# Kernel tuning notes

Measured on AMD Instinct MI355X. Metric: run time of the kernel, lower is better.

## Reference

```python
import jax, jax.numpy as jnp
import numpy as np

NUM_HEADS = 16
D_MODEL = 1024
D_K = 64
D_V = 64
NEG_INF = -1e9


def setup_inputs() -> dict:
    key = jax.random.key(0)
    ks = jax.random.split(key, 7)
    B, S = 2, 2048
    Q = jax.random.normal(ks[0], (B, S, D_MODEL), dtype=jnp.float32)
    K = jax.random.normal(ks[1], (B, S, D_MODEL), dtype=jnp.float32)
    V = jax.random.normal(ks[2], (B, S, D_MODEL), dtype=jnp.float32)
    s = 1.0 / np.sqrt(D_MODEL)
    W_q = jax.random.normal(ks[3], (D_MODEL, D_K * NUM_HEADS), dtype=jnp.float32) * s
    W_k = jax.random.normal(ks[4], (D_MODEL, D_K), dtype=jnp.float32) * s
    W_v = jax.random.normal(ks[5], (D_MODEL, D_V), dtype=jnp.float32) * s
    W_o = jax.random.normal(ks[6], (D_V * NUM_HEADS, D_MODEL), dtype=jnp.float32) * (1.0 / np.sqrt(D_V * NUM_HEADS))
    return {"Q": Q, "K": K, "V": V, "W_q": W_q, "W_k": W_k, "W_v": W_v, "W_o": W_o}


def reference(Q, K, V, W_q, W_k, W_v, W_o):
    B, Sq, _ = Q.shape
    Sk = K.shape[1]
    # projections: Q -> per-head, K/V -> single shared head (MQA)
    q = (Q @ W_q).reshape(B, Sq, NUM_HEADS, D_K).transpose(0, 2, 1, 3)  # [B,H,Sq,Dk]
    k = K @ W_k  # [B,Sk,Dk]
    v = V @ W_v  # [B,Sk,Dv]
    scores = jnp.einsum('bhqd,bkd->bhqk', q, k) / jnp.sqrt(jnp.float32(D_K))
    causal = jnp.tril(jnp.ones((Sq, Sk), dtype=bool))  # [Sq,Sk]
    scores = jnp.where(causal[None, None], scores, NEG_INF)
    attn = jax.nn.softmax(scores, axis=-1)  # [B,H,Sq,Sk]
    out = jnp.einsum('bhqk,bkd->bhqd', attn, v)  # [B,H,Sq,Dv]
    out = out.transpose(0, 2, 1, 3).reshape(B, Sq, NUM_HEADS * D_V)
    return out @ W_o
```

## Files before the change

### kernel.cpp

```cpp
#include <hip/hip_runtime.h>
#include <hip/hip_bf16.h>
#include <cstdint>

typedef __bf16 bf16_t;
typedef __bf16 bf16x8 __attribute__((ext_vector_type(8)));
typedef __bf16 bf16x4 __attribute__((ext_vector_type(4)));
typedef float  floatx4 __attribute__((ext_vector_type(4)));

__device__ __forceinline__ bf16_t f2bf(float x) { return (bf16_t)x; }

__device__ __forceinline__ void gll16(const void* g, void* l) {
  __builtin_amdgcn_global_load_lds((const __attribute__((address_space(1))) void*)g,
                                   (__attribute__((address_space(3))) void*)l, 16, 0, 0);
}

#define S_LEN 2048
#define NHEAD 16

__global__ __launch_bounds__(256) void transpose_all(const float* __restrict__ Wq,
                                                     const float* __restrict__ Wo,
                                                     const float* __restrict__ Wk,
                                                     const float* __restrict__ Wv,
                                                     bf16_t* __restrict__ Wqt,
                                                     bf16_t* __restrict__ Wot,
                                                     bf16_t* __restrict__ Wkt,
                                                     bf16_t* __restrict__ Wvt) {
  const int bid = blockIdx.x;
  const float* W; bf16_t* Wt; int n0, k0, N;
  if (bid < 2048) {
    int z = bid >> 10, rem = bid & 1023;
    W = z ? Wo : Wq; Wt = z ? Wot : Wqt;
    n0 = (rem & 31) * 32; k0 = (rem >> 5) * 32; N = 1024;
  } else {
    int b2 = bid - 2048, z = b2 >> 6, rem = b2 & 63;
    W = z ? Wv : Wk; Wt = z ? Wvt : Wkt;
    n0 = (rem & 1) * 32; k0 = (rem >> 1) * 32; N = 64;
  }
  const int K = 1024;
  __shared__ float tile[32][33];
  int tx = threadIdx.x & 31, ty = threadIdx.x >> 5;
#pragma unroll
  for (int r = 0; r < 4; ++r)
    tile[ty + 8 * r][tx] = W[(size_t)(k0 + ty + 8 * r) * N + n0 + tx];
  __syncthreads();
#pragma unroll
  for (int r = 0; r < 4; ++r)
    Wt[(size_t)(n0 + ty + 8 * r) * K + k0 + tx] = f2bf(tile[tx][ty + 8 * r]);
}

template <int OUTMODE, bool A_FP32>
__device__ __forceinline__ void gemm_body(const void* __restrict__ Ain,
                                          const bf16_t* __restrict__ Bt,
                                          void* __restrict__ Cout,
                                          int M, int N, int K,
                                          int m0, int n0,
                                          bf16_t* As, bf16_t* Bs) {
  constexpr int BK = 64;
  const int tid = threadIdx.x;
  const int wave = tid >> 6, lane = tid & 63;
  const int quad = lane >> 4, lm = lane & 15;
  const int wr = wave >> 1, wc = wave & 1;

  floatx4 acc[2][4];
#pragma unroll
  for (int i = 0; i < 2; ++i)
#pragma unroll
    for (int j = 0; j < 4; ++j) acc[i][j] = (floatx4){0.f, 0.f, 0.f, 0.f};

  for (int k0 = 0; k0 < K; k0 += BK) {
    if constexpr (A_FP32) {
#pragma unroll
      for (int rd = 0; rd < 2; ++rd) {
        int idx = rd * 256 + tid, row = idx >> 3, ch = (idx & 7) ^ (row & 7);
        const float* src = (const float*)Ain + (size_t)(m0 + row) * K + k0 + ch * 8;
        float4 f0 = *(const float4*)src;
        float4 f1 = *(const float4*)(src + 4);
        bf16x8 o;
        o[0] = f2bf(f0.x); o[1] = f2bf(f0.y); o[2] = f2bf(f0.z); o[3] = f2bf(f0.w);
        o[4] = f2bf(f1.x); o[5] = f2bf(f1.y); o[6] = f2bf(f1.z); o[7] = f2bf(f1.w);
        *(bf16x8*)&As[idx * 8] = o;
      }
    } else {
#pragma unroll
      for (int rd = 0; rd < 2; ++rd) {
        int idx = rd * 256 + tid, row = idx >> 3, ch = (idx & 7) ^ (row & 7);
        gll16((const bf16_t*)Ain + (size_t)(m0 + row) * K + k0 + ch * 8,
              As + (rd * 256 + wave * 64) * 8);
      }
    }
#pragma unroll
    for (int rd = 0; rd < 4; ++rd) {
      int idx = rd * 256 + tid, row = idx >> 3, ch = (idx & 7) ^ (row & 7);
      gll16(Bt + (size_t)(n0 + row) * K + k0 + ch * 8,
            Bs + (rd * 256 + wave * 64) * 8);
    }
    __syncthreads();
    const int sw = lm & 7;
    bf16x8 af[2][2], bfr[4][2];
#pragma unroll
    for (int i = 0; i < 2; ++i) {
      const bf16_t* base = &As[(wr * 32 + i * 16 + lm) * BK];
      af[i][0] = *(const bf16x8*)(base + ((quad ^ sw) * 8));
      af[i][1] = *(const bf16x8*)(base + (((4 + quad) ^ sw) * 8));
    }
#pragma unroll
    for (int j = 0; j < 4; ++j) {
      const bf16_t* base = &Bs[(wc * 64 + j * 16 + lm) * BK];
      bfr[j][0] = *(const bf16x8*)(base + ((quad ^ sw) * 8));
      bfr[j][1] = *(const bf16x8*)(base + (((4 + quad) ^ sw) * 8));
    }
#pragma unroll
    for (int ks = 0; ks < 2; ++ks)
#pragma unroll
      for (int i = 0; i < 2; ++i)
#pragma unroll
        for (int j = 0; j < 4; ++j)
          acc[i][j] = __builtin_amdgcn_mfma_f32_16x16x32_bf16(af[i][ks], bfr[j][ks],
                                                              acc[i][j], 0, 0, 0);
    __syncthreads();
  }
#pragma unroll
  for (int i = 0; i < 2; ++i) {
#pragma unroll
    for (int j = 0; j < 4; ++j) {
      int row0 = m0 + wr * 32 + i * 16 + quad * 4;
      int col = n0 + wc * 64 + j * 16 + lm;
#pragma unroll
      for (int r = 0; r < 4; ++r) {
        if constexpr (OUTMODE == 3)
          ((bf16_t*)Cout)[(size_t)(row0 + r) * N + col] = f2bf(acc[i][j][r] * 0.125f);
        else
          ((float*)Cout)[(size_t)(row0 + r) * N + col] = acc[i][j][r];
      }
    }
  }
}

__device__ __forceinline__ void kv_body(const float* __restrict__ A32,
                                        const bf16_t* __restrict__ Bt,
                                        bf16_t* __restrict__ kp,
                                        bf16_t* __restrict__ vpt,
                                        int M, int K, int m0, int isV,
                                        bf16_t* As, bf16_t* Bs) {
  constexpr int BK = 32, LDK = 40, N = 64;
  const int tid = threadIdx.x;
  const int wave = tid >> 6, lane = tid & 63;
  const int quad = lane >> 4, lm = lane & 15;
  const int wr = wave >> 1, wc = wave & 1;

  floatx4 acc[2][2];
#pragma unroll
  for (int i = 0; i < 2; ++i)
#pragma unroll
    for (int j = 0; j < 2; ++j) acc[i][j] = (floatx4){0.f, 0.f, 0.f, 0.f};

  for (int k0 = 0; k0 < K; k0 += BK) {
    {
      int row = tid >> 2, c8 = tid & 3;
      const float* src = A32 + (size_t)(m0 + row) * K + k0 + c8 * 8;
      float4 f0 = *(const float4*)src;
      float4 f1 = *(const float4*)(src + 4);
      bf16x8 o;
      o[0] = f2bf(f0.x); o[1] = f2bf(f0.y); o[2] = f2bf(f0.z); o[3] = f2bf(f0.w);
      o[4] = f2bf(f1.x); o[5] = f2bf(f1.y); o[6] = f2bf(f1.z); o[7] = f2bf(f1.w);
      *(bf16x8*)&As[row * LDK + c8 * 8] = o;
    }
    {
      int row = tid >> 2, c8 = tid & 3;
      *(bf16x8*)&Bs[row * LDK + c8 * 8] =
          *(const bf16x8*)(Bt + (size_t)row * K + k0 + c8 * 8);
    }
    __syncthreads();
    bf16x8 af[2], bfr[2];
#pragma unroll
    for (int i = 0; i < 2; ++i)
      af[i] = *(const bf16x8*)&As[(wr * 32 + i * 16 + lm) * LDK + quad * 8];
#pragma unroll
    for (int j = 0; j < 2; ++j)
      bfr[j] = *(const bf16x8*)&Bs[(wc * 32 + j * 16 + lm) * LDK + quad * 8];
#pragma unroll
    for (int i = 0; i < 2; ++i)
#pragma unroll
      for (int j = 0; j < 2; ++j)
        acc[i][j] = __builtin_amdgcn_mfma_f32_16x16x32_bf16(af[i], bfr[j],
                                                            acc[i][j], 0, 0, 0);
    __syncthreads();
  }
#pragma unroll
  for (int i = 0; i < 2; ++i) {
#pragma unroll
    for (int j = 0; j < 2; ++j) {
      int row0 = m0 + wr * 32 + i * 16 + quad * 4;
      int col = wc * 32 + j * 16 + lm;
      if (isV) {
        bf16x4 o;
#pragma unroll
        for (int r = 0; r < 4; ++r) o[r] = f2bf(acc[i][j][r]);
        *(bf16x4*)&vpt[(size_t)col * M + row0] = o;
      } else {
#pragma unroll
        for (int r = 0; r < 4; ++r)
          kp[(size_t)(row0 + r) * N + col] = f2bf(acc[i][j][r]);
      }
    }
  }
}

__global__ __launch_bounds__(256, 2) void proj_all(const float* __restrict__ Q,
                                                   const float* __restrict__ K,
                                                   const float* __restrict__ V,
                                                   const bf16_t* __restrict__ Wqt,
                                                   const bf16_t* __restrict__ Wkt,
                                                   const bf16_t* __restrict__ Wvt,
                                                   bf16_t* __restrict__ qp,
                                                   bf16_t* __restrict__ kp,
                                                   bf16_t* __restrict__ vpt,
                                                   int BS) {
  __shared__ __align__(16) bf16_t As[64 * 64];
  __shared__ __align__(16) bf16_t Bs[128 * 64];
  const int bid = blockIdx.x;
  const int nQ = (BS / 64) * 8;
  if (bid < nQ) {
    int m0 = (bid & (BS / 64 - 1)) * 64, n0 = (bid / (BS / 64)) * 128;
    gemm_body<3, true>(Q, Wqt, qp, BS, 1024, 1024, m0, n0, As, Bs);
  } else {
    int b2 = bid - nQ;
    int isV = (b2 >= BS / 64);
    int m0 = (b2 & (BS / 64 - 1)) * 64;
    kv_body(isV ? V : K, isV ? Wvt : Wkt, kp, vpt, BS, 1024, m0, isV, As, Bs);
  }
}

__global__ __launch_bounds__(256, 2) void gemm_oproj(const bf16_t* __restrict__ A,
                                                     const bf16_t* __restrict__ Bt,
                                                     float* __restrict__ Cout,
                                                     int M, int N, int K) {
  __shared__ __align__(16) bf16_t As[64 * 64];
  __shared__ __align__(16) bf16_t Bs[128 * 64];
  gemm_body<0, false>(A, Bt, Cout, M, N, K,
                      blockIdx.x * 64, blockIdx.y * 128, As, Bs);
}

__global__ __launch_bounds__(256, 2) void flash_mqa(const bf16_t* __restrict__ q,
                                                    const bf16_t* __restrict__ kk,
                                                    const bf16_t* __restrict__ vt,
                                                    bf16_t* __restrict__ O,
                                                    int BStot) {
  const int qt = 63 - blockIdx.x;
  const int hg = blockIdx.y, b = blockIdx.z;
  const int tid = threadIdx.x;
  const int wave = tid >> 6, lane = tid & 63;
  const int quad = lane >> 4, lm = lane & 15;
  const int h = hg * 4 + wave;

  __shared__ __align__(16) bf16_t k_lds[2][64 * 64];
  __shared__ __align__(16) bf16_t v_lds[2][64 * 64];
  __shared__ __align__(16) bf16_t p_lds[4][32 * 64];

  const size_t bS = (size_t)b * S_LEN;
  const int qb = qt * 32;
  const int ktmax = qt >> 1;
  const int qoff = qb - ktmax * 64;
  const int sw = lm & 7;

  bf16x8 qf[2][2];
#pragma unroll
  for (int m = 0; m < 2; ++m) {
    const bf16_t* qp = q + (bS + qb + m * 16 + lm) * 1024 + h * 64;
    qf[m][0] = *(const bf16x8*)(qp + quad * 8);
    qf[m][1] = *(const bf16x8*)(qp + 32 + quad * 8);
  }
  bf16x8 onesf;
#pragma unroll
  for (int j = 0; j < 8; ++j) onesf[j] = f2bf(1.0f);

  floatx4 acc[2][4];
  floatx4 ps[2];
#pragma unroll
  for (int m = 0; m < 2; ++m) {
    ps[m] = (floatx4){0.f, 0.f, 0.f, 0.f};
#pragma unroll
    for (int t = 0; t < 4; ++t) acc[m][t] = (floatx4){0.f, 0.f, 0.f, 0.f};
  }

  bf16x8 kst[2], vst[2];
  auto load_kv = [&](int kt) {
    const int k0 = kt * 64;
#pragma unroll
    for (int it = 0; it < 2; ++it) {
      int idx = it * 256 + tid, r = idx >> 3, c8 = idx & 7;
      kst[it] = *(const bf16x8*)(kk + (bS + k0 + r) * 64 + c8 * 8);
      vst[it] = *(const bf16x8*)(vt + (size_t)r * BStot + bS + k0 + c8 * 8);
    }
  };
  auto write_kv = [&](int buf) {
#pragma unroll
    for (int it = 0; it < 2; ++it) {
      int idx = it * 256 + tid, r = idx >> 3, c8 = idx & 7;
      int addr = r * 64 + ((c8 ^ (r & 7)) * 8);
      *(bf16x8*)&k_lds[buf][addr] = kst[it];
      *(bf16x8*)&v_lds[buf][addr] = vst[it];
    }
  };

  load_kv(0);
  write_kv(0);
  __syncthreads();

  for (int kt = 0; kt <= ktmax; ++kt) {
    const int cur = kt & 1;
    if (kt < ktmax) load_kv(kt + 1);
    const bool diag = (kt == ktmax);

#pragma unroll
    for (int t = 0; t < 4; ++t) {
      const bf16_t* kb = &k_lds[cur][(t * 16 + lm) * 64];
      bf16x8 a0 = *(const bf16x8*)(kb + ((quad ^ sw) * 8));
      bf16x8 a1 = *(const bf16x8*)(kb + (((4 + quad) ^ sw) * 8));
      floatx4 s[2];
#pragma unroll
      for (int m = 0; m < 2; ++m) {
        floatx4 cc = (floatx4){0.f, 0.f, 0.f, 0.f};
        cc = __builtin_amdgcn_mfma_f32_16x16x32_bf16(a0, qf[m][0], cc, 0, 0, 0);
        cc = __builtin_amdgcn_mfma_f32_16x16x32_bf16(a1, qf[m][1], cc, 0, 0, 0);
        s[m] = cc;
      }
      if (diag) {
#pragma unroll
        for (int m = 0; m < 2; ++m) {
          int qq = qoff + m * 16 + lm;
#pragma unroll
          for (int r = 0; r < 4; ++r) {
            int kj = t * 16 + quad * 4 + r;
            s[m][r] = (kj <= qq) ? __expf(s[m][r]) : 0.f;
          }
        }
      } else {
#pragma unroll
        for (int m = 0; m < 2; ++m)
#pragma unroll
          for (int r = 0; r < 4; ++r) s[m][r] = __expf(s[m][r]);
      }
#pragma unroll
      for (int m = 0; m < 2; ++m) {
        bf16x4 pk;
#pragma unroll
        for (int r = 0; r < 4; ++r) pk[r] = f2bf(s[m][r]);
        *(bf16x4*)&p_lds[wave][(m * 16 + lm) * 64 +
                               (((2 * t + (quad >> 1)) ^ sw) * 8) + (quad & 1) * 4] = pk;
      }
    }
    bf16x8 p0[2], p1[2];
#pragma unroll
    for (int m = 0; m < 2; ++m) {
      const bf16_t* pb = &p_lds[wave][(m * 16 + lm) * 64];
      p0[m] = *(const bf16x8*)(pb + ((quad ^ sw) * 8));
      p1[m] = *(const bf16x8*)(pb + (((4 + quad) ^ sw) * 8));
      ps[m] = __builtin_amdgcn_mfma_f32_16x16x32_bf16(p0[m], onesf, ps[m], 0, 0, 0);
      ps[m] = __builtin_amdgcn_mfma_f32_16x16x32_bf16(p1[m], onesf, ps[m], 0, 0, 0);
    }
#pragma unroll
    for (int t = 0; t < 4; ++t) {
      const bf16_t* vb = &v_lds[cur][(t * 16 + lm) * 64];
      bf16x8 v0 = *(const bf16x8*)(vb + ((quad ^ sw) * 8));
      bf16x8 v1 = *(const bf16x8*)(vb + (((4 + quad) ^ sw) * 8));
#pragma unroll
      for (int m = 0; m < 2; ++m) {
        acc[m][t] = __builtin_amdgcn_mfma_f32_16x16x32_bf16(p0[m], v0, acc[m][t], 0, 0, 0);
        acc[m][t] = __builtin_amdgcn_mfma_f32_16x16x32_bf16(p1[m], v1, acc[m][t], 0, 0, 0);
      }
    }
    if (kt < ktmax) write_kv(1 - cur);
    __syncthreads();
  }

#pragma unroll
  for (int m = 0; m < 2; ++m) {
    float rl[4];
#pragma unroll
    for (int r = 0; r < 4; ++r) rl[r] = 1.0f / ps[m][r];
    const int q0 = qb + m * 16 + quad * 4;
#pragma unroll
    for (int t = 0; t < 4; ++t)
#pragma unroll
      for (int r = 0; r < 4; ++r)
        O[(bS + q0 + r) * 1024 + h * 64 + t * 16 + lm] = f2bf(acc[m][t][r] * rl[r]);
  }
}

extern "C" void kernel_launch(void* const* d_in, const int* in_sizes, int n_in,
                              void* d_out, int out_size, void* d_ws, size_t ws_size,
                              hipStream_t stream) {
  const float* Q  = (const float*)d_in[0];
  const float* K  = (const float*)d_in[1];
  const float* V  = (const float*)d_in[2];
  const float* Wq = (const float*)d_in[3];
  const float* Wk = (const float*)d_in[4];
  const float* Wv = (const float*)d_in[5];
  const float* Wo = (const float*)d_in[6];

  const int BS = in_sizes[0] / 1024;
  const int B  = BS / S_LEN;

  bf16_t* ws  = (bf16_t*)d_ws;
  bf16_t* qp  = ws;
  bf16_t* Ob  = qp  + (size_t)BS * 1024;
  bf16_t* Wqt = Ob  + (size_t)BS * 1024;
  bf16_t* Wot = Wqt + (size_t)1024 * 1024;
  bf16_t* Wkt = Wot + (size_t)1024 * 1024;
  bf16_t* Wvt = Wkt + (size_t)64 * 1024;
  bf16_t* kp  = Wvt + (size_t)64 * 1024;
  bf16_t* vpt = kp  + (size_t)BS * 64;

  transpose_all<<<2176, 256, 0, stream>>>(Wq, Wo, Wk, Wv, Wqt, Wot, Wkt, Wvt);

  proj_all<<<(BS / 64) * 8 + (BS / 64) * 2, 256, 0, stream>>>(
      Q, K, V, Wqt, Wkt, Wvt, qp, kp, vpt, BS);

  flash_mqa<<<dim3(S_LEN / 32, NHEAD / 4, B), 256, 0, stream>>>(qp, kp, vpt, Ob, BS);

  gemm_oproj<<<dim3(BS / 64, 8), 256, 0, stream>>>(Ob, Wot, (float*)d_out, BS, 1024, 1024);
}
```

Measured before the change: 197.9 us.

## Split causal flash-MQA along the key axis and combine partials in separate kernel

Rather than one block per 32-row query tile walking all of its key tiles, each query tile is split into up to four chunks of eight key tiles. Each chunk writes unnormalized bf16 partial outputs and row sums to workspace, and a new combine kernel adds them and normalizes. The aim is to balance the causal triangle's uneven work across 160x4x2 blocks and shorten the tail set by the longest query tiles. In exchange it adds partial-output traffic (four bf16 slots of BSx1024), zero-fill writes for unused slots, an extra launch, and bf16 rounding of the partial sums. Skipping the running max is safe only because the chunks share no max rescaling.

```diff
diff --git a/kernel.cpp b/kernel.cpp
--- a/kernel.cpp
+++ b/kernel.cpp
@@ -244,9 +244,21 @@
 __global__ __launch_bounds__(256, 2) void flash_mqa(const bf16_t* __restrict__ q,
                                                     const bf16_t* __restrict__ kk,
                                                     const bf16_t* __restrict__ vt,
-                                                    bf16_t* __restrict__ O,
+                                                    bf16_t* __restrict__ Opart,
+                                                    float* __restrict__ lpart,
                                                     int BStot) {
-  const int qt = 63 - blockIdx.x;
+  const int c = blockIdx.x;
+  int qt, s;
+  if (c < 16)      { qt = c; s = 0; }
+  else if (c < 48) { qt = 16 + ((c - 16) >> 1); s = (c - 16) & 1; }
+  else if (c < 96) { int d = c - 48; int q3 = d / 3; qt = 32 + q3; s = d - q3 * 3; }
+  else             { qt = 48 + ((c - 96) >> 2); s = (c - 96) & 3; }
+  const int n = (qt >> 1) + 1;
+  const int nchunks = (n + 7) >> 3;
+  const int kt0 = s * 8;
+  const int kt1 = (kt0 + 8 < n) ? kt0 + 8 : n;
+  const int ktmax = n - 1;
+
   const int hg = blockIdx.y, b = blockIdx.z;
   const int tid = threadIdx.x;
   const int wave = tid >> 6, lane = tid & 63;
@@ -259,7 +271,6 @@
 
   const size_t bS = (size_t)b * S_LEN;
   const int qb = qt * 32;
-  const int ktmax = qt >> 1;
   const int qoff = qb - ktmax * 64;
   const int sw = lm & 7;
 
@@ -303,13 +314,13 @@
     }
   };
 
-  load_kv(0);
-  write_kv(0);
+  load_kv(kt0);
+  write_kv(kt0 & 1);
   __syncthreads();
 
-  for (int kt = 0; kt <= ktmax; ++kt) {
+  for (int kt = kt0; kt < kt1; ++kt) {
     const int cur = kt & 1;
-    if (kt < ktmax) load_kv(kt + 1);
+    if (kt + 1 < kt1) load_kv(kt + 1);
     const bool diag = (kt == ktmax);
 
 #pragma unroll
@@ -317,13 +328,13 @@
       const bf16_t* kb = &k_lds[cur][(t * 16 + lm) * 64];
       bf16x8 a0 = *(const bf16x8*)(kb + ((quad ^ sw) * 8));
       bf16x8 a1 = *(const bf16x8*)(kb + (((4 + quad) ^ sw) * 8));
-      floatx4 s[2];
+      floatx4 sv[2];
 #pragma unroll
       for (int m = 0; m < 2; ++m) {
         floatx4 cc = (floatx4){0.f, 0.f, 0.f, 0.f};
         cc = __builtin_amdgcn_mfma_f32_16x16x32_bf16(a0, qf[m][0], cc, 0, 0, 0);
         cc = __builtin_amdgcn_mfma_f32_16x16x32_bf16(a1, qf[m][1], cc, 0, 0, 0);
-        s[m] = cc;
+        sv[m] = cc;
       }
       if (diag) {
 #pragma unroll
@@ -332,20 +343,20 @@
 #pragma unroll
           for (int r = 0; r < 4; ++r) {
             int kj = t * 16 + quad * 4 + r;
-            s[m][r] = (kj <= qq) ? __expf(s[m][r]) : 0.f;
+            sv[m][r] = (kj <= qq) ? __expf(sv[m][r]) : 0.f;
           }
         }
       } else {
 #pragma unroll
         for (int m = 0; m < 2; ++m)
 #pragma unroll
-          for (int r = 0; r < 4; ++r) s[m][r] = __expf(s[m][r]);
+          for (int r = 0; r < 4; ++r) sv[m][r] = __expf(sv[m][r]);
       }
 #pragma unroll
       for (int m = 0; m < 2; ++m) {
         bf16x4 pk;
 #pragma unroll
-        for (int r = 0; r < 4; ++r) pk[r] = f2bf(s[m][r]);
+        for (int r = 0; r < 4; ++r) pk[r] = f2bf(sv[m][r]);
         *(bf16x4*)&p_lds[wave][(m * 16 + lm) * 64 +
                                (((2 * t + (quad >> 1)) ^ sw) * 8) + (quad & 1) * 4] = pk;
       }
@@ -370,22 +381,69 @@
         acc[m][t] = __builtin_amdgcn_mfma_f32_16x16x32_bf16(p1[m], v1, acc[m][t], 0, 0, 0);
       }
     }
-    if (kt < ktmax) write_kv(1 - cur);
+    if (kt + 1 < kt1) write_kv(1 - cur);
     __syncthreads();
   }
 
+  const size_t slotO = (size_t)BStot * 1024;
+  const size_t slotL = (size_t)BStot * 16;
 #pragma unroll
   for (int m = 0; m < 2; ++m) {
-    float rl[4];
-#pragma unroll
-    for (int r = 0; r < 4; ++r) rl[r] = 1.0f / ps[m][r];
     const int q0 = qb + m * 16 + quad * 4;
 #pragma unroll
     for (int t = 0; t < 4; ++t)
 #pragma unroll
       for (int r = 0; r < 4; ++r)
-        O[(bS + q0 + r) * 1024 + h * 64 + t * 16 + lm] = f2bf(acc[m][t][r] * rl[r]);
-  }
+        Opart[s * slotO + (bS + q0 + r) * 1024 + h * 64 + t * 16 + lm] =
+            f2bf(acc[m][t][r]);
+    if (lm == 0)
+#pragma unroll
+      for (int r = 0; r < 4; ++r)
+        lpart[s * slotL + (bS + q0 + r) * 16 + h] = ps[m][r];
+  }
+  if (s == 0) {
+    for (int ss = nchunks; ss < 4; ++ss) {
+#pragma unroll
+      for (int m = 0; m < 2; ++m) {
+        const int q0 = qb + m * 16 + quad * 4;
+#pragma unroll
+        for (int t = 0; t < 4; ++t)
+#pragma unroll
+          for (int r = 0; r < 4; ++r)
+            Opart[ss * slotO + (bS + q0 + r) * 1024 + h * 64 + t * 16 + lm] = f2bf(0.f);
+        if (lm == 0)
+#pragma unroll
+          for (int r = 0; r < 4; ++r)
+            lpart[ss * slotL + (bS + q0 + r) * 16 + h] = 0.f;
+      }
+    }
+  }
+}
+
+__global__ __launch_bounds__(256) void combine_o(const bf16_t* __restrict__ Opart,
+                                                 const float* __restrict__ lpart,
+                                                 bf16_t* __restrict__ Ob, int BS) {
+  const int idx = (blockIdx.x * 256 + threadIdx.x) * 8;
+  const int row = idx >> 10, col = idx & 1023, h = col >> 6;
+  const size_t slotO = (size_t)BS * 1024;
+  const size_t slotL = (size_t)BS * 16;
+  float l = 0.f;
+#pragma unroll
+  for (int s = 0; s < 4; ++s) l += lpart[s * slotL + row * 16 + h];
+  float o[8];
+#pragma unroll
+  for (int j = 0; j < 8; ++j) o[j] = 0.f;
+#pragma unroll
+  for (int s = 0; s < 4; ++s) {
+    bf16x8 v = *(const bf16x8*)(Opart + s * slotO + idx);
+#pragma unroll
+    for (int j = 0; j < 8; ++j) o[j] += (float)v[j];
+  }
+  const float rl = 1.0f / l;
+  bf16x8 out;
+#pragma unroll
+  for (int j = 0; j < 8; ++j) out[j] = f2bf(o[j] * rl);
+  *(bf16x8*)(Ob + idx) = out;
 }
 
 extern "C" void kernel_launch(void* const* d_in, const int* in_sizes, int n_in,
@@ -411,13 +469,17 @@
   bf16_t* Wvt = Wkt + (size_t)64 * 1024;
   bf16_t* kp  = Wvt + (size_t)64 * 1024;
   bf16_t* vpt = kp  + (size_t)BS * 64;
+  bf16_t* Opart = vpt + (size_t)BS * 64;
+  float*  lpart = (float*)(Opart + (size_t)4 * BS * 1024);
 
   transpose_all<<<2176, 256, 0, stream>>>(Wq, Wo, Wk, Wv, Wqt, Wot, Wkt, Wvt);
 
   proj_all<<<(BS / 64) * 8 + (BS / 64) * 2, 256, 0, stream>>>(
       Q, K, V, Wqt, Wkt, Wvt, qp, kp, vpt, BS);
 
-  flash_mqa<<<dim3(S_LEN / 32, NHEAD / 4, B), 256, 0, stream>>>(qp, kp, vpt, Ob, BS);
+  flash_mqa<<<dim3(160, NHEAD / 4, B), 256, 0, stream>>>(qp, kp, vpt, Opart, lpart, BS);
+
+  combine_o<<<(BS * 1024) / (256 * 8), 256, 0, stream>>>(Opart, lpart, Ob, BS);
 
   gemm_oproj<<<dim3(BS / 64, 8), 256, 0, stream>>>(Ob, Wot, (float*)d_out, BS, 1024, 1024);
 }
```

Result: faster. 192.8 us (-2.6%).
